# Performance work log

Hardware: AMD Instinct MI355X
Metric: run time of the kernel (lower is better)

The kernel has to match this reference:

```python
import jax, jax.numpy as jnp
import numpy as np

B, T, C, H = 8, 1024, 768, 12
HD = C // H  # 64, even for RoPE
ROPE_THETA = 10000.0


def precompute_freqs_cis(dim, end, theta=ROPE_THETA):
    # [end, dim//2, 2] with (cos, sin) in last axis
    freqs = 1.0 / theta ** (jnp.arange(0, dim // 2).astype(jnp.float32) / (dim // 2))
    t = jnp.arange(end)
    f = jnp.outer(t, freqs)
    return jnp.stack([jnp.cos(f), jnp.sin(f)], axis=-1)


def apply_rope(x, fc):
    # x: [B,T,H,hd]; fc: [T,1,hd//2,2] (broadcasts over B and H)
    xr = x.reshape(*x.shape[:-1], -1, 2)
    x_re, x_im = xr[..., 0], xr[..., 1]
    cos, sin = fc[..., 0], fc[..., 1]
    out_re = x_re * cos - x_im * sin
    out_im = x_re * sin + x_im * cos
    return jnp.stack([out_re, out_im], axis=-1).reshape(x.shape)


def setup_inputs() -> dict:
    key = jax.random.key(0)
    k0, k1, k2 = jax.random.split(key, 3)
    x = jax.random.normal(k0, (B, T, C), jnp.float32)
    Wqkv = jax.random.normal(k1, (C, 3 * C), jnp.float32) * 0.02
    bqkv = jnp.zeros((3 * C,), jnp.float32)
    Wproj = jax.random.normal(k2, (C, C), jnp.float32) * 0.02
    bproj = jnp.zeros((C,), jnp.float32)
    mask = jnp.tril(jnp.ones((T, T), jnp.int32))  # causal
    return {"x": x, "Wqkv": Wqkv, "bqkv": bqkv, "Wproj": Wproj, "bproj": bproj, "mask": mask}


def reference(x, Wqkv, bqkv, Wproj, bproj, mask):
    B_, T_, C_ = x.shape
    qkv = (x @ Wqkv + bqkv).reshape(B_, T_, 3, H, HD)
    q, k, v = qkv[:, :, 0], qkv[:, :, 1], qkv[:, :, 2]  # each [B,T,H,hd]
    fc = precompute_freqs_cis(HD, T_)[:, None]  # [T,1,hd//2,2]
    q = apply_rope(q, fc)
    k = apply_rope(k, fc)
    scale = 1.0 / jnp.sqrt(jnp.float32(HD))
    attn = jnp.einsum('bthd,bkhd->bhtk', q, k) * scale  # [B,H,T,T]
    neg = jnp.finfo(attn.dtype).min
    attn = jnp.where(mask[None, None, :, :] == 0, neg, attn)
    attn = jax.nn.softmax(attn, axis=-1)
    out = jnp.einsum('bhtk,bkhd->bthd', attn, v).reshape(B_, T_, C_)
    return out @ Wproj + bproj
```

## Files before the change

kernel.cpp:

```cpp
#include <hip/hip_runtime.h>
#include <cstdint>
#include <cstddef>
#include <cstring>

#define BB 8
#define TT 1024
#define CC 768
#define NH 12
#define HD 64

using bf16x8 = __attribute__((ext_vector_type(8))) short;
using f32x4  = __attribute__((ext_vector_type(4))) float;

static __device__ __forceinline__ short f2bf(float f) {
    uint32_t u;
    __builtin_memcpy(&u, &f, 4);
    u += 0x7FFFu + ((u >> 16) & 1u);
    return (short)(u >> 16);
}

static __device__ __forceinline__ uint32_t bfpack(float lo, float hi) {
    return (uint32_t)(uint16_t)f2bf(lo) | ((uint32_t)(uint16_t)f2bf(hi) << 16);
}

__global__ __launch_bounds__(256)
void prep_kernel(const float* __restrict__ x, const float* __restrict__ Wqkv,
                 const float* __restrict__ Wproj,
                 short* __restrict__ WqkvT, short* __restrict__ WprojT,
                 short* __restrict__ xb, float2* __restrict__ fc) {
    __shared__ float tile[32][33];
    const int tid = threadIdx.x;
    int bid = blockIdx.x;
    if (bid < 2304) {
        const float* in;
        short* out;
        int Cdim, bx, by;
        if (bid < 1728) { in = Wqkv; out = WqkvT; Cdim = 2304; bx = bid % 72; by = bid / 72; }
        else { int b2 = bid - 1728; in = Wproj; out = WprojT; Cdim = 768; bx = b2 % 24; by = b2 / 24; }
        int tx = tid & 31, ty = tid >> 5;
        int c0 = bx * 32, r0 = by * 32;
#pragma unroll
        for (int i = 0; i < 4; i++)
            tile[ty + 8 * i][tx] = in[(size_t)(r0 + ty + 8 * i) * Cdim + c0 + tx];
        __syncthreads();
#pragma unroll
        for (int i = 0; i < 4; i++)
            out[(size_t)(c0 + ty + 8 * i) * 768 + r0 + tx] = f2bf(tile[tx][ty + 8 * i]);
    } else if (bid < 5376) {
        int i = ((bid - 2304) * 256 + tid) * 8;
        float4 f0 = *(const float4*)(x + i);
        float4 f1 = *(const float4*)(x + i + 4);
        bf16x8 h;
        h[0] = f2bf(f0.x); h[1] = f2bf(f0.y); h[2] = f2bf(f0.z); h[3] = f2bf(f0.w);
        h[4] = f2bf(f1.x); h[5] = f2bf(f1.y); h[6] = f2bf(f1.z); h[7] = f2bf(f1.w);
        *(bf16x8*)(xb + i) = h;
    } else {
        int idx = (bid - 5376) * 256 + tid;
        int t = idx >> 5, p = idx & 31;
        float freq = powf(10000.0f, -(float)p / 32.0f);
        float a = (float)t * freq;
        fc[idx] = make_float2(cosf(a), sinf(a));
    }
}

template <int EPI>
__global__ __launch_bounds__(256, 2)
void gemm_kernel(const short* __restrict__ Agl, const short* __restrict__ BT,
                 const float* __restrict__ bias,
                 short* __restrict__ Qb, short* __restrict__ Kb, short* __restrict__ VT,
                 const float2* __restrict__ fc, float* __restrict__ out) {
    __shared__ __align__(16) short smem_s[4 * 128 * 64];
    short (*As)[128 * 64] = (short(*)[128 * 64])smem_s;
    short (*Bs)[128 * 64] = (short(*)[128 * 64])(smem_s + 2 * 128 * 64);
    const int tid = threadIdx.x;
    const int lane = tid & 63, wid = tid >> 6;
    const int g = lane >> 4, c = lane & 15;
    const int wm = wid >> 1, wn = wid & 1;

    const int nx = gridDim.x;
    const int bid = blockIdx.y * nx + blockIdx.x;
    const int cpx = (nx * gridDim.y) >> 3;
    const int swz = (bid & 7) * cpx + (bid >> 3);
    const int m0 = (swz / nx) * 128, n0 = (swz % nx) * 128;

    const int srow = lane >> 2;
    const int sch = lane & 3;
    const short* Ab0 = Agl + (size_t)(m0 + wid * 32 + srow) * 768 + sch * 8;
    const short* Bb0 = BT  + (size_t)(n0 + wid * 32 + srow) * 768 + sch * 8;

    const f32x4 zero4 = {0.f, 0.f, 0.f, 0.f};
    f32x4 acc[4][4];
#pragma unroll
    for (int i = 0; i < 4; i++)
#pragma unroll
        for (int j = 0; j < 4; j++) acc[i][j] = zero4;

    bf16x8 rA[4], rB[4];
#define LOAD(kt)                                                               \
    {                                                                          \
        size_t ko = (size_t)(kt) * 64;                                         \
        _Pragma("unroll")                                                      \
        for (int q = 0; q < 2; q++)                                            \
            _Pragma("unroll")                                                  \
            for (int h = 0; h < 2; h++) {                                      \
                rA[q * 2 + h] = *(const bf16x8*)(Ab0 + (size_t)q * 16 * 768 + ko + h * 32); \
                rB[q * 2 + h] = *(const bf16x8*)(Bb0 + (size_t)q * 16 * 768 + ko + h * 32); \
            }                                                                  \
    }
#define WRITE(buf)                                                             \
    {                                                                          \
        _Pragma("unroll")                                                      \
        for (int q = 0; q < 2; q++)                                            \
            _Pragma("unroll")                                                  \
            for (int h = 0; h < 2; h++) {                                      \
                int row = wid * 32 + q * 16 + srow;                            \
                int ci = sch + h * 4;                                          \
                int idx = row * 64 + ((ci ^ (row & 7)) * 8);                   \
                *(bf16x8*)&As[buf][idx] = rA[q * 2 + h];                       \
                *(bf16x8*)&Bs[buf][idx] = rB[q * 2 + h];                       \
            }                                                                  \
    }
#define COMPUTE(buf)                                                           \
    {                                                                          \
        _Pragma("unroll")                                                      \
        for (int kk = 0; kk < 2; kk++) {                                       \
            bf16x8 af[4], bfr[4];                                              \
            _Pragma("unroll")                                                  \
            for (int mi = 0; mi < 4; mi++) {                                   \
                int row = wm * 64 + mi * 16 + c;                               \
                af[mi] = *(const bf16x8*)&As[buf][row * 64 + (((kk * 4 + g) ^ (row & 7)) * 8)]; \
            }                                                                  \
            _Pragma("unroll")                                                  \
            for (int ni = 0; ni < 4; ni++) {                                   \
                int row = wn * 64 + ni * 16 + c;                               \
                bfr[ni] = *(const bf16x8*)&Bs[buf][row * 64 + (((kk * 4 + g) ^ (row & 7)) * 8)]; \
            }                                                                  \
            __builtin_amdgcn_s_setprio(1);                                     \
            _Pragma("unroll")                                                  \
            for (int mi = 0; mi < 4; mi++)                                     \
                _Pragma("unroll")                                              \
                for (int ni = 0; ni < 4; ni++)                                 \
                    acc[mi][ni] = __builtin_amdgcn_mfma_f32_16x16x32_bf16(     \
                        af[mi], bfr[ni], acc[mi][ni], 0, 0, 0);                \
            __builtin_amdgcn_s_setprio(0);                                     \
        }                                                                      \
    }

    LOAD(0);
    WRITE(0);
    __syncthreads();

#pragma unroll 1
    for (int t2 = 0; t2 < 12; t2 += 2) {
        LOAD(t2 + 1);
        COMPUTE(0);
        __syncthreads();
        WRITE(1);
        __syncthreads();
        if (t2 + 2 < 12) {
            LOAD(t2 + 2);
            COMPUTE(1);
            __syncthreads();
            WRITE(0);
            __syncthreads();
        } else {
            COMPUTE(1);
        }
    }
    __syncthreads();

    if (EPI == 0) {
        uint32_t* LD = (uint32_t*)smem_s;
#pragma unroll
        for (int ni = 0; ni < 4; ni++) {
            int nl = wn * 64 + ni * 16 + c;
            int n = n0 + nl;
            float bv = bias[n];
            int part = (n >= 1536) ? 2 : (n >= 768 ? 1 : 0);
            int d = (n - part * 768) & 63;
#pragma unroll
            for (int mi = 0; mi < 4; mi++) {
#pragma unroll
                for (int r = 0; r < 4; r++) {
                    int ml = wm * 64 + mi * 16 + g * 4 + r;
                    float v = acc[mi][ni][r] + bv;
                    float pv = __shfl_xor(v, 1);
                    if (!(c & 1)) {
                        float o0, o1;
                        if (part < 2) {
                            int t = (m0 + ml) & 1023;
                            float2 cs = fc[t * 32 + (d >> 1)];
                            o0 = v * cs.x - pv * cs.y;
                            o1 = v * cs.y + pv * cs.x;
                            if (part == 0) { o0 *= 0.125f; o1 *= 0.125f; }
                        } else { o0 = v; o1 = pv; }
                        LD[ml * 64 + ((nl >> 1) ^ (((ml >> 2) & 3) << 3))] = bfpack(o0, o1);
                    }
                }
            }
        }
        __syncthreads();
        if (n0 >= 1536) {
            int n0r = n0 - 1536;
            int h0 = n0r >> 6;
            int wc = tid & 63;
            int seg = tid >> 2 >> 4;
            int h = h0 + (wc >> 5);
            int d0 = (2 * wc) & 63;
            int b = m0 >> 10, t0r = m0 & 1023;
            uint32_t wlo[16], whi[16];
#pragma unroll
            for (int j2 = 0; j2 < 16; j2++) {
                int mlA = seg * 32 + 2 * j2;
                int mlB = mlA + 1;
                uint32_t wa = LD[mlA * 64 + (wc ^ (((mlA >> 2) & 3) << 3))];
                uint32_t wb = LD[mlB * 64 + (wc ^ (((mlB >> 2) & 3) << 3))];
                wlo[j2] = (wa & 0xFFFFu) | (wb << 16);
                whi[j2] = (wa >> 16) | (wb & 0xFFFF0000u);
            }
            short* p0 = VT + ((size_t)(b * NH + h) * HD + d0) * TT + t0r + seg * 32;
            short* p1 = p0 + TT;
#pragma unroll
            for (int k = 0; k < 4; k++) {
                int4 v0, v1;
                __builtin_memcpy(&v0, &wlo[k * 4], 16);
                __builtin_memcpy(&v1, &whi[k * 4], 16);
                *(int4*)(p0 + k * 8) = v0;
                *(int4*)(p1 + k * 8) = v1;
            }
        } else {
#pragma unroll
            for (int p = 0; p < 8; p++) {
                int ml = p * 16 + (tid >> 4);
                int wc = (tid & 15) * 4;
                int4 dat = *(const int4*)&LD[ml * 64 + (wc ^ (((ml >> 2) & 3) << 3))];
                int n = n0 + wc * 2;
                int part = (n >= 768) ? 1 : 0;
                int rem = n - part * 768;
                int h = rem >> 6, d = rem & 63;
                int m = m0 + ml, b = m >> 10, t = m & 1023;
                short* dst = (part == 0 ? Qb : Kb)
                             + (((size_t)b * NH + h) * TT + t) * HD + d;
                *(int4*)dst = dat;
            }
        }
    } else {
        float* LDf = (float*)smem_s;
#pragma unroll
        for (int mi = 0; mi < 4; mi++)
#pragma unroll
            for (int ni = 0; ni < 4; ni++) {
                int nl = wn * 64 + ni * 16 + c;
                float bv = bias[n0 + nl];
#pragma unroll
                for (int r = 0; r < 4; r++) {
                    int ml = wm * 64 + mi * 16 + g * 4 + r;
                    LDf[ml * 128 + (nl ^ (r << 3))] = acc[mi][ni][r] + bv;
                }
            }
        __syncthreads();
#pragma unroll
        for (int p = 0; p < 8; p++) {
            int ml = p * 16 + (tid >> 4);
            int rr = (ml & 3) << 3;
            int wc4 = (tid & 15) * 8;
            const float* rp = &LDf[ml * 128 + (wc4 ^ rr)];
            float4 f0 = *(const float4*)rp;
            float4 f1 = *(const float4*)(rp + 4);
            float* dst = out + (size_t)(m0 + ml) * CC + n0 + wc4;
            *(float4*)dst = f0;
            *(float4*)(dst + 4) = f1;
        }
    }
#undef LOAD
#undef WRITE
#undef COMPUTE
}

__global__ __launch_bounds__(256)
void attn_kernel(const short* __restrict__ Qb, const short* __restrict__ Kb,
                 const short* __restrict__ VT, short* __restrict__ Ob) {
    __shared__ uint32_t Pt[4][32][32];
    __shared__ uint32_t ot[128 * 32];
    const int tid = threadIdx.x, lane = tid & 63, wid = tid >> 6;
    const int g = lane >> 4, c = lane & 15;
    const int bh = blockIdx.x, qb = 7 - (int)blockIdx.y;
    const int b = bh / NH, h = bh % NH;
    const short* Qp = Qb + (size_t)bh * TT * HD;
    const short* Kp = Kb + (size_t)bh * TT * HD;
    const short* Vp = VT + (size_t)bh * TT * HD;
    const int q0 = qb * 128 + wid * 32;
    const int sw = (c & 7) << 2;

    bf16x8 qf[2][2];
#pragma unroll
    for (int qs = 0; qs < 2; qs++)
#pragma unroll
        for (int kh = 0; kh < 2; kh++)
            qf[qs][kh] = *(const bf16x8*)(Qp + (size_t)(q0 + qs * 16 + c) * HD + kh * 32 + g * 8);

    const f32x4 zero4 = {0.f, 0.f, 0.f, 0.f};
    f32x4 o[2][4];
#pragma unroll
    for (int qs = 0; qs < 2; qs++)
#pragma unroll
        for (int dt = 0; dt < 4; dt++) o[qs][dt] = zero4;
    float mrun[2] = {-1e30f, -1e30f}, lrun[2] = {0.f, 0.f};

    const int t0max = ((q0 + 31) >> 6) << 6;
    for (int t0 = 0; t0 <= t0max; t0 += 64) {
        f32x4 st[2][4];
#pragma unroll
        for (int nt = 0; nt < 4; nt++) {
            const short* kp = Kp + (size_t)(t0 + nt * 16 + c) * HD + g * 8;
            bf16x8 k0 = *(const bf16x8*)kp;
            bf16x8 k1 = *(const bf16x8*)(kp + 32);
#pragma unroll
            for (int qs = 0; qs < 2; qs++) {
                f32x4 z = zero4;
                z = __builtin_amdgcn_mfma_f32_16x16x32_bf16(k0, qf[qs][0], z, 0, 0, 0);
                z = __builtin_amdgcn_mfma_f32_16x16x32_bf16(k1, qf[qs][1], z, 0, 0, 0);
                st[qs][nt] = z;
            }
        }
        bf16x8 vf[2][4];
#pragma unroll
        for (int blk = 0; blk < 2; blk++)
#pragma unroll
            for (int dt = 0; dt < 4; dt++)
                vf[blk][dt] = *(const bf16x8*)(Vp + (size_t)(dt * 16 + c) * TT + t0 + blk * 32 + g * 8);
        if (t0 + 63 > q0) {
#pragma unroll
            for (int qs = 0; qs < 2; qs++) {
                int q = q0 + qs * 16 + c;
#pragma unroll
                for (int nt = 0; nt < 4; nt++)
#pragma unroll
                    for (int r = 0; r < 4; r++)
                        if (t0 + nt * 16 + g * 4 + r > q) st[qs][nt][r] = -1e30f;
            }
        }
#pragma unroll
        for (int qs = 0; qs < 2; qs++) {
            float mx = st[qs][0][0];
#pragma unroll
            for (int nt = 0; nt < 4; nt++)
#pragma unroll
                for (int r = 0; r < 4; r++) mx = fmaxf(mx, st[qs][nt][r]);
            mx = fmaxf(mx, __shfl_xor(mx, 16));
            mx = fmaxf(mx, __shfl_xor(mx, 32));
            float mnew = fmaxf(mrun[qs], mx);
            float al = __expf(mrun[qs] - mnew);
            mrun[qs] = mnew;
            float sm = 0.f;
#pragma unroll
            for (int nt = 0; nt < 4; nt++)
#pragma unroll
                for (int r = 0; r < 4; r++) {
                    float e = __expf(st[qs][nt][r] - mnew);
                    st[qs][nt][r] = e;
                    sm += e;
                }
            sm += __shfl_xor(sm, 16);
            sm += __shfl_xor(sm, 32);
            lrun[qs] = lrun[qs] * al + sm;
#pragma unroll
            for (int dt = 0; dt < 4; dt++) {
                o[qs][dt][0] *= al; o[qs][dt][1] *= al;
                o[qs][dt][2] *= al; o[qs][dt][3] *= al;
            }
            int row = qs * 16 + c;
#pragma unroll
            for (int nt = 0; nt < 4; nt++) {
                uint32_t w0 = bfpack(st[qs][nt][0], st[qs][nt][1]);
                uint32_t w1 = bfpack(st[qs][nt][2], st[qs][nt][3]);
                int wa = nt * 8 + 2 * g;
                Pt[wid][row][wa ^ sw]       = w0;
                Pt[wid][row][(wa + 1) ^ sw] = w1;
            }
        }
#pragma unroll
        for (int qs = 0; qs < 2; qs++) {
            int row = qs * 16 + c;
#pragma unroll
            for (int blk = 0; blk < 2; blk++) {
                bf16x8 pf = *(const bf16x8*)&Pt[wid][row][(blk * 16 + 4 * g) ^ sw];
#pragma unroll
                for (int dt = 0; dt < 4; dt++)
                    o[qs][dt] = __builtin_amdgcn_mfma_f32_16x16x32_bf16(
                        vf[blk][dt], pf, o[qs][dt], 0, 0, 0);
            }
        }
    }

#pragma unroll
    for (int qs = 0; qs < 2; qs++) {
        float inv = 1.0f / lrun[qs];
        int ql = wid * 32 + qs * 16 + c;
#pragma unroll
        for (int dt = 0; dt < 4; dt++) {
            uint32_t w0 = bfpack(o[qs][dt][0] * inv, o[qs][dt][1] * inv);
            uint32_t w1 = bfpack(o[qs][dt][2] * inv, o[qs][dt][3] * inv);
            int jc0 = dt * 8 + 2 * g;
            int jc1 = jc0 + 1;
            ot[ql * 32 + ((((jc0 >> 2) ^ (c & 7)) << 2) | (jc0 & 3))] = w0;
            ot[ql * 32 + ((((jc1 >> 2) ^ (c & 7)) << 2) | (jc1 & 3))] = w1;
        }
    }
    __syncthreads();
#pragma unroll
    for (int p = 0; p < 4; p++) {
        int q = (tid >> 3) + 32 * p;
        int jb = tid & 7;
        const uint32_t* src = &ot[q * 32 + ((jb ^ (q & 7)) << 2)];
        int4 w = *(const int4*)src;
        *(int4*)(Ob + ((size_t)b * TT + qb * 128 + q) * CC + h * HD + jb * 8) = w;
    }
}

extern "C" void kernel_launch(void* const* d_in, const int* in_sizes, int n_in,
                              void* d_out, int out_size, void* d_ws, size_t ws_size,
                              hipStream_t stream) {
    const float* x     = (const float*)d_in[0];
    const float* Wqkv  = (const float*)d_in[1];
    const float* bqkv  = (const float*)d_in[2];
    const float* Wproj = (const float*)d_in[3];
    const float* bproj = (const float*)d_in[4];

    char* ws = (char*)d_ws;
    short*  WqkvT  = (short*)(ws);
    short*  WprojT = (short*)(ws + 3538944);
    float2* fc     = (float2*)(ws + 3538944 + 1179648);
    short*  Qb     = (short*)(ws + 4980736);
    short*  Kb     = (short*)(ws + 4980736 + 1 * 12582912);
    short*  VOb    = (short*)(ws + 4980736 + 2 * 12582912);
    short*  VbT    = (short*)(ws + 4980736 + 3 * 12582912);
    short*  xb     = VOb;
    float*  out    = (float*)d_out;

    hipLaunchKernelGGL(prep_kernel, dim3(5504), dim3(256), 0, stream,
                       x, Wqkv, Wproj, WqkvT, WprojT, xb, fc);
    hipLaunchKernelGGL((gemm_kernel<0>), dim3(18, 64), dim3(256), 0, stream,
                       xb, WqkvT, bqkv, Qb, Kb, VbT, fc, (float*)nullptr);
    hipLaunchKernelGGL(attn_kernel, dim3(96, 8), dim3(256), 0, stream, Qb, Kb, VbT, VOb);
    hipLaunchKernelGGL((gemm_kernel<1>), dim3(6, 64), dim3(256), 0, stream,
                       VOb, WprojT, bproj,
                       (short*)nullptr, (short*)nullptr, (short*)nullptr,
                       (const float2*)nullptr, out);
}
```

Baseline: 163.2 us.

## Process 128-key tiles per softmax step in attention, reuse P buffer for output

The attention inner loop now handles two 64-key blocks per iteration, so the online-softmax max/sum reductions, shuffles and accumulator rescaling run once per 128 keys. A 64-key tail iteration covers the remainder. The P staging buffer is widened to 64 words per row and reused, after a barrier, as the output transpose buffer, which keeps total LDS use unchanged. In exchange, V loads move after the softmax instead of overlapping the QK MFMAs, and holding two score tiles raises register pressure.

```diff
diff --git a/kernel.cpp b/kernel.cpp
--- a/kernel.cpp
+++ b/kernel.cpp
@@ -280,8 +280,7 @@
 __global__ __launch_bounds__(256)
 void attn_kernel(const short* __restrict__ Qb, const short* __restrict__ Kb,
                  const short* __restrict__ VT, short* __restrict__ Ob) {
-    __shared__ uint32_t Pt[4][32][32];
-    __shared__ uint32_t ot[128 * 32];
+    __shared__ uint32_t Pt[4][32][64];
     const int tid = threadIdx.x, lane = tid & 63, wid = tid >> 6;
     const int g = lane >> 4, c = lane & 15;
     const int bh = blockIdx.x, qb = 7 - (int)blockIdx.y;
@@ -307,9 +306,11 @@
         for (int dt = 0; dt < 4; dt++) o[qs][dt] = zero4;
     float mrun[2] = {-1e30f, -1e30f}, lrun[2] = {0.f, 0.f};
 
-    const int t0max = ((q0 + 31) >> 6) << 6;
-    for (int t0 = 0; t0 <= t0max; t0 += 64) {
-        f32x4 st[2][4];
+    const int end = (((q0 + 31) >> 6) << 6) + 64;
+    int t0 = 0;
+
+    for (; t0 + 128 <= end; t0 += 128) {
+        f32x4 sta[2][4], stb[2][4];
 #pragma unroll
         for (int nt = 0; nt < 4; nt++) {
             const short* kp = Kp + (size_t)(t0 + nt * 16 + c) * HD + g * 8;
@@ -320,15 +321,126 @@
                 f32x4 z = zero4;
                 z = __builtin_amdgcn_mfma_f32_16x16x32_bf16(k0, qf[qs][0], z, 0, 0, 0);
                 z = __builtin_amdgcn_mfma_f32_16x16x32_bf16(k1, qf[qs][1], z, 0, 0, 0);
+                sta[qs][nt] = z;
+            }
+        }
+#pragma unroll
+        for (int nt = 0; nt < 4; nt++) {
+            const short* kp = Kp + (size_t)(t0 + 64 + nt * 16 + c) * HD + g * 8;
+            bf16x8 k0 = *(const bf16x8*)kp;
+            bf16x8 k1 = *(const bf16x8*)(kp + 32);
+#pragma unroll
+            for (int qs = 0; qs < 2; qs++) {
+                f32x4 z = zero4;
+                z = __builtin_amdgcn_mfma_f32_16x16x32_bf16(k0, qf[qs][0], z, 0, 0, 0);
+                z = __builtin_amdgcn_mfma_f32_16x16x32_bf16(k1, qf[qs][1], z, 0, 0, 0);
+                stb[qs][nt] = z;
+            }
+        }
+        if (t0 + 63 > q0) {
+#pragma unroll
+            for (int qs = 0; qs < 2; qs++) {
+                int q = q0 + qs * 16 + c;
+#pragma unroll
+                for (int nt = 0; nt < 4; nt++)
+#pragma unroll
+                    for (int r = 0; r < 4; r++)
+                        if (t0 + nt * 16 + g * 4 + r > q) sta[qs][nt][r] = -1e30f;
+            }
+        }
+        if (t0 + 127 > q0) {
+#pragma unroll
+            for (int qs = 0; qs < 2; qs++) {
+                int q = q0 + qs * 16 + c;
+#pragma unroll
+                for (int nt = 0; nt < 4; nt++)
+#pragma unroll
+                    for (int r = 0; r < 4; r++)
+                        if (t0 + 64 + nt * 16 + g * 4 + r > q) stb[qs][nt][r] = -1e30f;
+            }
+        }
+#pragma unroll
+        for (int qs = 0; qs < 2; qs++) {
+            float mx = sta[qs][0][0];
+#pragma unroll
+            for (int nt = 0; nt < 4; nt++)
+#pragma unroll
+                for (int r = 0; r < 4; r++) {
+                    mx = fmaxf(mx, sta[qs][nt][r]);
+                    mx = fmaxf(mx, stb[qs][nt][r]);
+                }
+            mx = fmaxf(mx, __shfl_xor(mx, 16));
+            mx = fmaxf(mx, __shfl_xor(mx, 32));
+            float mnew = fmaxf(mrun[qs], mx);
+            float al = __expf(mrun[qs] - mnew);
+            mrun[qs] = mnew;
+            float sm = 0.f;
+#pragma unroll
+            for (int nt = 0; nt < 4; nt++)
+#pragma unroll
+                for (int r = 0; r < 4; r++) {
+                    float ea = __expf(sta[qs][nt][r] - mnew);
+                    sta[qs][nt][r] = ea; sm += ea;
+                    float eb = __expf(stb[qs][nt][r] - mnew);
+                    stb[qs][nt][r] = eb; sm += eb;
+                }
+            sm += __shfl_xor(sm, 16);
+            sm += __shfl_xor(sm, 32);
+            lrun[qs] = lrun[qs] * al + sm;
+#pragma unroll
+            for (int dt = 0; dt < 4; dt++) {
+                o[qs][dt][0] *= al; o[qs][dt][1] *= al;
+                o[qs][dt][2] *= al; o[qs][dt][3] *= al;
+            }
+            int row = qs * 16 + c;
+#pragma unroll
+            for (int nt = 0; nt < 4; nt++) {
+                int wa = nt * 8 + 2 * g;
+                Pt[wid][row][wa ^ sw]            = bfpack(sta[qs][nt][0], sta[qs][nt][1]);
+                Pt[wid][row][(wa + 1) ^ sw]      = bfpack(sta[qs][nt][2], sta[qs][nt][3]);
+                Pt[wid][row][32 + (wa ^ sw)]     = bfpack(stb[qs][nt][0], stb[qs][nt][1]);
+                Pt[wid][row][32 + ((wa + 1) ^ sw)] = bfpack(stb[qs][nt][2], stb[qs][nt][3]);
+            }
+        }
+#pragma unroll
+        for (int half = 0; half < 2; half++) {
+            bf16x8 vf[2][4];
+#pragma unroll
+            for (int blk = 0; blk < 2; blk++)
+#pragma unroll
+                for (int dt = 0; dt < 4; dt++)
+                    vf[blk][dt] = *(const bf16x8*)(Vp + (size_t)(dt * 16 + c) * TT +
+                                                   t0 + half * 64 + blk * 32 + g * 8);
+#pragma unroll
+            for (int qs = 0; qs < 2; qs++) {
+                int row = qs * 16 + c;
+#pragma unroll
+                for (int blk = 0; blk < 2; blk++) {
+                    bf16x8 pf = *(const bf16x8*)&Pt[wid][row][half * 32 + ((blk * 16 + 4 * g) ^ sw)];
+#pragma unroll
+                    for (int dt = 0; dt < 4; dt++)
+                        o[qs][dt] = __builtin_amdgcn_mfma_f32_16x16x32_bf16(
+                            vf[blk][dt], pf, o[qs][dt], 0, 0, 0);
+                }
+            }
+        }
+    }
+
+    if (t0 < end) {
+        f32x4 st[2][4];
+#pragma unroll
+        for (int nt = 0; nt < 4; nt++) {
+            const short* kp = Kp + (size_t)(t0 + nt * 16 + c) * HD + g * 8;
+            bf16x8 k0 = *(const bf16x8*)kp;
+            bf16x8 k1 = *(const bf16x8*)(kp + 32);
+#pragma unroll
+            for (int qs = 0; qs < 2; qs++) {
+                f32x4 z = zero4;
+                z = __builtin_amdgcn_mfma_f32_16x16x32_bf16(k0, qf[qs][0], z, 0, 0, 0);
+                z = __builtin_amdgcn_mfma_f32_16x16x32_bf16(k1, qf[qs][1], z, 0, 0, 0);
                 st[qs][nt] = z;
             }
         }
-        bf16x8 vf[2][4];
-#pragma unroll
-        for (int blk = 0; blk < 2; blk++)
-#pragma unroll
-            for (int dt = 0; dt < 4; dt++)
-                vf[blk][dt] = *(const bf16x8*)(Vp + (size_t)(dt * 16 + c) * TT + t0 + blk * 32 + g * 8);
         if (t0 + 63 > q0) {
 #pragma unroll
             for (int qs = 0; qs < 2; qs++) {
@@ -372,13 +484,17 @@
             int row = qs * 16 + c;
 #pragma unroll
             for (int nt = 0; nt < 4; nt++) {
-                uint32_t w0 = bfpack(st[qs][nt][0], st[qs][nt][1]);
-                uint32_t w1 = bfpack(st[qs][nt][2], st[qs][nt][3]);
                 int wa = nt * 8 + 2 * g;
-                Pt[wid][row][wa ^ sw]       = w0;
-                Pt[wid][row][(wa + 1) ^ sw] = w1;
-            }
-        }
+                Pt[wid][row][wa ^ sw]       = bfpack(st[qs][nt][0], st[qs][nt][1]);
+                Pt[wid][row][(wa + 1) ^ sw] = bfpack(st[qs][nt][2], st[qs][nt][3]);
+            }
+        }
+        bf16x8 vf[2][4];
+#pragma unroll
+        for (int blk = 0; blk < 2; blk++)
+#pragma unroll
+            for (int dt = 0; dt < 4; dt++)
+                vf[blk][dt] = *(const bf16x8*)(Vp + (size_t)(dt * 16 + c) * TT + t0 + blk * 32 + g * 8);
 #pragma unroll
         for (int qs = 0; qs < 2; qs++) {
             int row = qs * 16 + c;
@@ -393,6 +509,8 @@
         }
     }
 
+    __syncthreads();
+    uint32_t* ot = &Pt[0][0][0];
 #pragma unroll
     for (int qs = 0; qs < 2; qs++) {
         float inv = 1.0f / lrun[qs];
```

Result: slower. 176.6 us (+8.2%).
